# Performance work log

Measured on AMD Instinct MI355X. Metric: run time of the kernel, lower is better.

The kernel has to match this reference:

```python
import jax, jax.numpy as jnp
import numpy as np

L, B, C, H = 1024, 8, 1024, 16
D = C // H  # 64


def setup_inputs() -> dict:
    key = jax.random.key(0)
    ks = jax.random.split(key, 8)
    hidden_states = jax.random.normal(ks[0], (L, B, C), dtype=jnp.float32)
    rotary_pos_emb = jax.random.uniform(ks[1], (L, D // 2), dtype=jnp.float32) * 10.0
    attention_mask = jax.random.randint(ks[2], (B, L, L), 0, 2) > 0
    s = 1.0 / np.sqrt(C)
    Wqkv = jax.random.uniform(ks[3], (3 * C, C), dtype=jnp.float32, minval=-s, maxval=s)
    bqkv = jax.random.uniform(ks[4], (3 * C,), dtype=jnp.float32, minval=-s, maxval=s)
    Wo = jax.random.uniform(ks[5], (C, C), dtype=jnp.float32, minval=-s, maxval=s)
    bo = jax.random.uniform(ks[6], (C,), dtype=jnp.float32, minval=-s, maxval=s)
    return {"hidden_states": hidden_states, "rotary_pos_emb": rotary_pos_emb,
            "attention_mask": attention_mask, "Wqkv": Wqkv, "bqkv": bqkv, "Wo": Wo, "bo": bo}


def _rotate_half(x):
    # interleaved pairs: [-x1, x0, -x3, x2, ...]
    x2 = x.reshape(*x.shape[:-1], -1, 2)
    return jnp.stack((-x2[..., 1], x2[..., 0]), axis=-1).reshape(x.shape)


def reference(hidden_states, rotary_pos_emb, attention_mask, Wqkv, bqkv, Wo, bo):
    Lx, Bx, Cx = hidden_states.shape
    # QKV projection: (L,B,3C) -> (3,B,L,H,D)
    qkv = hidden_states @ Wqkv.T + bqkv
    qkv = qkv.reshape(Lx, Bx, 3, H, D).transpose(2, 1, 0, 3, 4)
    q, k, v = qkv[0], qkv[1], qkv[2]  # (B, L, H, D)
    # RoPE: freqs (L, D/2) -> cos/sin (1, L, 1, D) via duplication
    rpe = rotary_pos_emb[None] if rotary_pos_emb.ndim == 2 else rotary_pos_emb
    cos = jnp.concatenate([jnp.cos(rpe), jnp.cos(rpe)], axis=-1)[:, :, None, :]
    sin = jnp.concatenate([jnp.sin(rpe), jnp.sin(rpe)], axis=-1)[:, :, None, :]
    q = q * cos + _rotate_half(q) * sin
    k = k * cos + _rotate_half(k) * sin
    # (B, H, L, D)
    q = q.transpose(0, 2, 1, 3)
    k = k.transpose(0, 2, 1, 3)
    v = v.transpose(0, 2, 1, 3)
    scale = 1.0 / jnp.sqrt(jnp.asarray(D, dtype=q.dtype))
    scores = jnp.einsum('bhqd,bhkd->bhqk', q, k) * scale
    # torch SDPA bool mask: True = attend, False = masked
    scores = jnp.where(attention_mask[:, None, :, :], scores, jnp.finfo(scores.dtype).min)
    attn = jax.nn.softmax(scores, axis=-1)
    out = jnp.einsum('bhqk,bhkd->bhqd', attn, v)  # (B, H, L, D)
    out = out.transpose(2, 0, 1, 3).reshape(Lx, Bx, Cx)  # (L, B, C)
    return out @ Wo.T + bo
```

## Files before the change

### kernel.cpp

```cpp
#include <hip/hip_runtime.h>
#include <hip/hip_bf16.h>

typedef short bf16x8 __attribute__((ext_vector_type(8)));
typedef short bf16x4 __attribute__((ext_vector_type(4)));
typedef float f32x4 __attribute__((ext_vector_type(4)));
typedef unsigned int u32;
typedef unsigned long long u64;

#define GLD_LDS16(gp, lp) \
  __builtin_amdgcn_global_load_lds((const __attribute__((address_space(1))) u32*)(gp), \
                                   (__attribute__((address_space(3))) u32*)(lp), 16, 0, 0)

__device__ __forceinline__ short f2bf(float f) {
  u32 u = __builtin_bit_cast(u32, f);
  u = (u + 0x7fffu + ((u >> 16) & 1u)) >> 16;
  return (short)u;
}

__device__ __forceinline__ u32 pack2_bf16(float a, float b) {
#if __has_builtin(__builtin_amdgcn_cvt_pk_bf16_f32)
  typedef __bf16 bf16v2 __attribute__((ext_vector_type(2)));
  bf16v2 r = __builtin_amdgcn_cvt_pk_bf16_f32(a, b);
  return __builtin_bit_cast(u32, r);
#else
  u32 r;
  asm("v_cvt_pk_bf16_f32 %0, %1, %2" : "=v"(r) : "v"(a), "v"(b));
  return r;
#endif
}

__device__ __forceinline__ float exp2_fast(float x) {
#if __has_builtin(__builtin_amdgcn_exp2f)
  return __builtin_amdgcn_exp2f(x);
#else
  return exp2f(x);
#endif
}

__global__ __launch_bounds__(256) void prep_all(
    const int* __restrict__ m, u64* __restrict__ maskb,
    const float* __restrict__ hs, const float* __restrict__ wqkv,
    const float* __restrict__ wo, short* __restrict__ xb,
    short* __restrict__ wqkvb, short* __restrict__ wob,
    const float* __restrict__ rpe, float* __restrict__ cosT,
    float* __restrict__ sinT) {
  int b = blockIdx.x;
  if (b < 32768) {
    int i = b * 256 + threadIdx.x;
    u64 bm = __ballot(m[i] != 0);
    if ((threadIdx.x & 63) == 0) maskb[i >> 6] = bm;
    return;
  }
  b -= 32768;
  if (b < 12288) {
    const float* in;
    short* out;
    int base;
    if (b < 8192) {
      in = hs; out = xb; base = b * 1024;
    } else if (b < 8192 + 3072) {
      in = wqkv; out = wqkvb; base = (b - 8192) * 1024;
    } else {
      in = wo; out = wob; base = (b - 11264) * 1024;
    }
    int i = base + threadIdx.x * 4;
    float4 v = *(const float4*)(in + i);
    short4 o;
    o.x = f2bf(v.x); o.y = f2bf(v.y); o.z = f2bf(v.z); o.w = f2bf(v.w);
    *(short4*)(out + i) = o;
    return;
  }
  b -= 12288;
  int i = b * 256 + threadIdx.x;
  float v = rpe[i];
  cosT[i] = cosf(v);
  sinT[i] = sinf(v);
}

__global__ __launch_bounds__(512, 2) void gemm_qkv(
    const short* __restrict__ Xb, const short* __restrict__ Wb,
    const float* __restrict__ bqkv, const float* __restrict__ cosT,
    const float* __restrict__ sinT, short* __restrict__ qb,
    short* __restrict__ kbuf, short* __restrict__ vbuf) {
  __shared__ short lds[3][24576];
  const int tid = threadIdx.x;
  const int wid = tid >> 6, lane = tid & 63;
  const int g = lane >> 4, c = lane & 15;
  const int wm = wid >> 2, wn = wid & 3;
  const int bid = blockIdx.y * 12 + blockIdx.x;
  const int swz = (bid & 7) * 96 + (bid >> 3);
  const int m0 = (swz / 12) * 128, n0 = (swz % 12) * 256;

  f32x4 acc[4][4];
#pragma unroll
  for (int i = 0; i < 4; i++)
#pragma unroll
    for (int j = 0; j < 4; j++) acc[i][j] = (f32x4){0.f, 0.f, 0.f, 0.f};

  const int trow = tid >> 3;
  const int gch = ((tid & 7) ^ (trow & 7)) * 8;
  const short* Ag = Xb + (long)(m0 + trow) * 1024 + gch;
  const short* Bg = Wb + (long)(n0 + trow) * 1024 + gch;
  const int lo = tid * 8;

  const int fA = (wm * 64 + c) * 64;
  const int fB = 8192 + (wn * 64 + c) * 64;
  const int ck0 = (g ^ (c & 7)) * 8;

#define QKV_STG_P0(bs, ko) do { \
    GLD_LDS16(Ag + (ko),             &lds[bs][lo]); \
    GLD_LDS16(Ag + (ko) + 64 * 1024, &lds[bs][4096 + lo]); \
    GLD_LDS16(Bg + (ko),             &lds[bs][8192 + lo]); \
  } while (0)
#define QKV_STG_P1(bs, ko) do { \
    GLD_LDS16(Bg + (ko) + 64 * 1024,  &lds[bs][12288 + lo]); \
    GLD_LDS16(Bg + (ko) + 128 * 1024, &lds[bs][16384 + lo]); \
    GLD_LDS16(Bg + (ko) + 192 * 1024, &lds[bs][20480 + lo]); \
  } while (0)

  QKV_STG_P0(0, 0);  QKV_STG_P1(0, 0);
  QKV_STG_P0(1, 64); QKV_STG_P1(1, 64);
  asm volatile("s_waitcnt vmcnt(6)" ::: "memory");
  __builtin_amdgcn_s_barrier();

  int bc = 0;
  for (int kt = 0; kt < 16; ++kt) {
    const short* Bf = &lds[bc][0];
    const int bs = (bc + 2 >= 3) ? bc - 1 : bc + 2;
    const int ko2 = (kt + 2) * 64;
    bf16x8 af[4], bfr[4];

#pragma unroll
    for (int mf = 0; mf < 4; mf++) af[mf] = *(const bf16x8*)&Bf[fA + mf * 1024 + ck0];
#pragma unroll
    for (int nf = 0; nf < 4; nf++) bfr[nf] = *(const bf16x8*)&Bf[fB + nf * 1024 + ck0];
    if (kt < 14) QKV_STG_P0(bs, ko2);
    __builtin_amdgcn_s_barrier();
    asm volatile("s_waitcnt lgkmcnt(0)" ::: "memory");
    __builtin_amdgcn_sched_barrier(0);
    __builtin_amdgcn_s_setprio(1);
#pragma unroll
    for (int mf = 0; mf < 4; mf++)
#pragma unroll
      for (int nf = 0; nf < 4; nf++)
        acc[mf][nf] = __builtin_amdgcn_mfma_f32_16x16x32_bf16(bfr[nf], af[mf], acc[mf][nf], 0, 0, 0);
    __builtin_amdgcn_s_setprio(0);
    __builtin_amdgcn_s_barrier();

#pragma unroll
    for (int mf = 0; mf < 4; mf++) af[mf] = *(const bf16x8*)&Bf[fA + mf * 1024 + (ck0 ^ 32)];
#pragma unroll
    for (int nf = 0; nf < 4; nf++) bfr[nf] = *(const bf16x8*)&Bf[fB + nf * 1024 + (ck0 ^ 32)];
    if (kt < 14) QKV_STG_P1(bs, ko2);
    __builtin_amdgcn_s_barrier();
    asm volatile("s_waitcnt lgkmcnt(0)" ::: "memory");
    __builtin_amdgcn_sched_barrier(0);
    __builtin_amdgcn_s_setprio(1);
#pragma unroll
    for (int mf = 0; mf < 4; mf++)
#pragma unroll
      for (int nf = 0; nf < 4; nf++)
        acc[mf][nf] = __builtin_amdgcn_mfma_f32_16x16x32_bf16(bfr[nf], af[mf], acc[mf][nf], 0, 0, 0);
    __builtin_amdgcn_s_setprio(0);
    if (kt < 14) {
      asm volatile("s_waitcnt vmcnt(6)" ::: "memory");
    } else if (kt == 14) {
      asm volatile("s_waitcnt vmcnt(0)" ::: "memory");
    }
    __builtin_amdgcn_s_barrier();
    bc = (bc + 1 == 3) ? 0 : bc + 1;
  }
#undef QKV_STG_P0
#undef QKV_STG_P1

  for (int jt = 0; jt < 4; jt++) {
    const int chan = n0 + wn * 64 + jt * 16 + g * 4;
    const int three = chan >> 10;
    const int hh = (chan >> 6) & 15;
    const int d = chan & 63;
    const float4 bq = *(const float4*)&bqkv[chan];
    for (int i = 0; i < 4; i++) {
      const int r = m0 + wm * 64 + i * 16 + c;
      const int l = r >> 3, b = r & 7;
      float v0 = acc[i][jt][0] + bq.x;
      float v1 = acc[i][jt][1] + bq.y;
      float v2 = acc[i][jt][2] + bq.z;
      float v3 = acc[i][jt][3] + bq.w;
      const long doff = ((long)(b * 16 + hh) * 1024 + l) * 64 + d;
      if (three == 2) {
        uint2 o = {pack2_bf16(v0, v1), pack2_bf16(v2, v3)};
        *(uint2*)&vbuf[doff] = o;
      } else {
        const float4 cs = *(const float4*)&cosT[l * 32 + (d & 31)];
        const float4 sn = *(const float4*)&sinT[l * 32 + (d & 31)];
        float e0 = v0 * cs.x - v1 * sn.x;
        float o0 = v1 * cs.y + v0 * sn.y;
        float e1 = v2 * cs.z - v3 * sn.z;
        float o1 = v3 * cs.w + v2 * sn.w;
        short* dst;
        if (three == 0) {
          const float S = 0.18033688011f;
          e0 *= S; o0 *= S; e1 *= S; o1 *= S;
          dst = qb;
        } else {
          dst = kbuf;
        }
        uint2 o = {pack2_bf16(e0, o0), pack2_bf16(e1, o1)};
        *(uint2*)&dst[doff] = o;
      }
    }
  }
}

__global__ __launch_bounds__(256) void transpose_v(const short* __restrict__ vbuf,
                                                   short* __restrict__ vTb) {
  __shared__ short T[64 * 72];
  const int bh = blockIdx.y;
  const int l0 = blockIdx.x * 64;
  const int t = threadIdx.x;
  const int row = t >> 3;
  const int cc = (t & 7) * 8;
  const short* src = vbuf + ((long)bh * 1024 + l0) * 64;
  for (int p = 0; p < 2; p++) {
    int lr = row + p * 32;
    *(bf16x8*)&T[lr * 72 + cc] = *(const bf16x8*)&src[(long)lr * 64 + cc];
  }
  __syncthreads();
  short* dst = vTb + (long)bh * 64 * 1024 + l0;
  for (int p = 0; p < 2; p++) {
    int d = row + p * 32;
    bf16x8 v;
    for (int j = 0; j < 8; j++) v[j] = T[(cc + j) * 72 + d];
    *(bf16x8*)&dst[(long)d * 1024 + cc] = v;
  }
}

__global__ __launch_bounds__(256, 5) void flash_attn(
    const short* __restrict__ qb, const short* __restrict__ kbuf,
    const short* __restrict__ vTb, const u64* __restrict__ maskb,
    short* __restrict__ attno) {
  __shared__ short K0[64 * 64], K1[64 * 64];
  __shared__ short V0[64 * 64], V1[64 * 64];
  const int t = threadIdx.x;
  const int wid = t >> 6, lane = t & 63;
  const int g = lane >> 4, c = lane & 15;
  const int bid = blockIdx.y * 16 + blockIdx.x;
  const int swz = (bid & 7) * 256 + (bid >> 3);
  const int q0 = (swz & 15) * 64;
  const int bh = swz >> 4;
  const int b = bh >> 4;
  const int h = bh & 15;
  const long qoff = (long)bh * 1024 * 64;
  const int qrow = q0 + wid * 16 + c;

  bf16x8 aq0, aq1;
  {
    const short* qp = qb + qoff + (long)qrow * 64;
    aq0 = *(const bf16x8*)(qp + g * 8);
    aq1 = *(const bf16x8*)(qp + 32 + g * 8);
  }

  f32x4 Od[4];
  for (int i = 0; i < 4; i++) Od[i] = (f32x4){0.f, 0.f, 0.f, 0.f};
  f32x4 Ld = (f32x4){0.f, 0.f, 0.f, 0.f};
  float m_run = -1e30f;

  bf16x8 avOnes8;
  {
    union { bf16x8 v; u32 u[4]; } av;
    u32 o1 = (c == 0) ? 0x3F803F80u : 0u;
    av.u[0] = av.u[1] = av.u[2] = av.u[3] = o1;
    avOnes8 = av.v;
  }

  const u64* mrow = maskb + ((long)b * 1024 + qrow) * 16;
  const short* Kg = kbuf + qoff;
  const short* Vg = vTb + qoff;

  const int l8 = lane >> 3, l7 = lane & 7;
  const int sr = wid * 16 + l8;
  const int sch = ((l7 ^ l8) & 7) * 8;
  const int r1 = wid * 16 + l8;
  const int r2 = r1 + 8;
  const int kp1 = (r1 & 32) | (((r1 & 15) >> 2) << 3) | (((r1 >> 4) & 1) << 2) | (r1 & 3);
  const int kp2 = (r2 & 32) | (((r2 & 15) >> 2) << 3) | (((r2 >> 4) & 1) << 2) | (r2 & 3);

  const int ck0 = g ^ (c & 7);
  const int kOff0 = c * 64 + ck0 * 8;
  const int kOff1 = c * 64 + (ck0 ^ 4) * 8;
  int vOff32[2];
  for (int kg = 0; kg < 2; kg++)
    vOff32[kg] = c * 64 + (((kg * 4 + g) ^ (c & 7)) * 8);

#define STAGE(KD, VD, ktn) do { \
    GLD_LDS16(Kg + (long)((ktn) + kp1) * 64 + sch,      &KD[(wid * 16) * 64]); \
    GLD_LDS16(Kg + (long)((ktn) + kp2) * 64 + sch,      &KD[(wid * 16 + 8) * 64]); \
    GLD_LDS16(Vg + (long)sr * 1024 + (ktn) + sch,       &VD[(wid * 16) * 64]); \
    GLD_LDS16(Vg + (long)(sr + 8) * 1024 + (ktn) + sch, &VD[(wid * 16 + 8) * 64]); \
  } while (0)

#define TILE(KB, VB, KP, VP, ki) do { \
    u64 mw = mrow[ki]; \
    __syncthreads(); \
    STAGE(KP, VP, (((ki) + 1) & 15) * 64); \
    f32x4 z[4]; \
    for (int nt = 0; nt < 4; nt++) { \
      bf16x8 bk0 = *(const bf16x8*)&KB[kOff0 + nt * 1024]; \
      bf16x8 bk1 = *(const bf16x8*)&KB[kOff1 + nt * 1024]; \
      f32x4 zz = (f32x4){0.f, 0.f, 0.f, 0.f}; \
      zz = __builtin_amdgcn_mfma_f32_16x16x32_bf16(bk0, aq0, zz, 0, 0, 0); \
      zz = __builtin_amdgcn_mfma_f32_16x16x32_bf16(bk1, aq1, zz, 0, 0, 0); \
      z[nt] = zz; \
    } \
    float mx = fmaxf(fmaxf(fmaxf(z[0][0], z[0][1]), fmaxf(z[0][2], z[0][3])), \
                     fmaxf(fmaxf(z[1][0], z[1][1]), fmaxf(z[1][2], z[1][3]))); \
    mx = fmaxf(mx, fmaxf(fmaxf(fmaxf(z[2][0], z[2][1]), fmaxf(z[2][2], z[2][3])), \
                         fmaxf(fmaxf(z[3][0], z[3][1]), fmaxf(z[3][2], z[3][3])))); \
    if (__ballot(mx > m_run + 8.f)) { \
      mx = fmaxf(mx, __shfl_xor(mx, 16, 64)); \
      mx = fmaxf(mx, __shfl_xor(mx, 32, 64)); \
      float mnew = fmaxf(m_run, mx); \
      float al = exp2_fast(m_run - mnew); \
      for (int dt = 0; dt < 4; dt++) { \
        Od[dt][0] *= al; Od[dt][1] *= al; Od[dt][2] *= al; Od[dt][3] *= al; \
      } \
      Ld[0] *= al; \
      m_run = mnew; \
    } \
    for (int kg = 0; kg < 2; kg++) { \
      union { bf16x8 v; u32 u[4]; } pu; \
      for (int ntp = 0; ntp < 2; ntp++) { \
        const int nt = kg * 2 + ntp; \
        u32 m4 = (u32)(mw >> (kg * 32 + g * 8 + ntp * 4)) & 0xFu; \
        u32 mlo = ((m4 & 1u) ? 0xFFFFu : 0u) | ((m4 & 2u) ? 0xFFFF0000u : 0u); \
        u32 mhi = ((m4 & 4u) ? 0xFFFFu : 0u) | ((m4 & 8u) ? 0xFFFF0000u : 0u); \
        float p0 = exp2_fast(z[nt][0] - m_run); \
        float p1 = exp2_fast(z[nt][1] - m_run); \
        float p2 = exp2_fast(z[nt][2] - m_run); \
        float p3 = exp2_fast(z[nt][3] - m_run); \
        pu.u[ntp * 2 + 0] = pack2_bf16(p0, p1) & mlo; \
        pu.u[ntp * 2 + 1] = pack2_bf16(p2, p3) & mhi; \
      } \
      Ld = __builtin_amdgcn_mfma_f32_16x16x32_bf16(avOnes8, pu.v, Ld, 0, 0, 0); \
      for (int dt = 0; dt < 4; dt++) { \
        bf16x8 av = *(const bf16x8*)&VB[vOff32[kg] + dt * 1024]; \
        Od[dt] = __builtin_amdgcn_mfma_f32_16x16x32_bf16(av, pu.v, Od[dt], 0, 0, 0); \
      } \
    } \
  } while (0)

  STAGE(K0, V0, 0);
  for (int ki = 0; ki < 16; ki += 2) {
    TILE(K0, V0, K1, V1, ki);
    TILE(K1, V1, K0, V0, ki + 1);
  }
#undef TILE
#undef STAGE

  float lsum = __shfl(Ld[0], c, 64);
  float inv = 1.f / lsum;
  long rbase = ((long)qrow * 8 + b) * 1024 + h * 64 + g * 4;
  for (int dt = 0; dt < 4; dt++) {
    union { bf16x4 v; u32 u[2]; } o;
    o.u[0] = pack2_bf16(Od[dt][0] * inv, Od[dt][1] * inv);
    o.u[1] = pack2_bf16(Od[dt][2] * inv, Od[dt][3] * inv);
    *(bf16x4*)&attno[rbase + dt * 16] = o.v;
  }
}

__global__ __launch_bounds__(256, 4) void gemm_out(
    const short* __restrict__ Ab, const short* __restrict__ Wob,
    const float* __restrict__ bo, float* __restrict__ out) {
  __shared__ short Ash[2][128 * 32];
  __shared__ short Bsh[2][128 * 32];
  const int tid = threadIdx.x;
  const int wid = tid >> 6, lane = tid & 63;
  const int g = lane >> 4, c = lane & 15;
  const int wm = wid >> 1, wn = wid & 1;
  const int bid = blockIdx.y * 8 + blockIdx.x;
  const int swz = (bid & 7) * 64 + (bid >> 3);
  const int m0 = (swz >> 3) * 128, n0 = (swz & 7) * 128;

  f32x4 acc[4][4];
  for (int i = 0; i < 4; i++)
    for (int j = 0; j < 4; j++) acc[i][j] = (f32x4){0.f, 0.f, 0.f, 0.f};

  const int srow = lane >> 2;
  const int scol = ((lane & 3) ^ ((lane >> 3) & 3)) * 8;
  const short* AgL = Ab + (long)(m0 + wid * 32 + srow) * 1024 + scol;
  const short* BgL = Wob + (long)(n0 + wid * 32 + srow) * 1024 + scol;
  const int dst0 = (wid * 32) * 32;
  const int dst1 = (wid * 32 + 16) * 32;
  const int ck = g ^ ((c >> 1) & 3);

#define OUT_STAGE(PA, PB, nko) do { \
    GLD_LDS16(AgL + (nko), &(PA)[dst0]); \
    GLD_LDS16(AgL + (nko) + 16 * 1024, &(PA)[dst1]); \
    GLD_LDS16(BgL + (nko), &(PB)[dst0]); \
    GLD_LDS16(BgL + (nko) + 16 * 1024, &(PB)[dst1]); \
  } while (0)

#define OUT_COMPUTE(CA, CB) do { \
    bf16x8 af[4], bfr[4]; \
    for (int i = 0; i < 4; i++) \
      af[i] = *(const bf16x8*)&(CA)[(wm * 64 + i * 16 + c) * 32 + ck * 8]; \
    for (int j = 0; j < 4; j++) \
      bfr[j] = *(const bf16x8*)&(CB)[(wn * 64 + j * 16 + c) * 32 + ck * 8]; \
    for (int i = 0; i < 4; i++) \
      for (int j = 0; j < 4; j++) \
        acc[i][j] = __builtin_amdgcn_mfma_f32_16x16x32_bf16(af[i], bfr[j], acc[i][j], 0, 0, 0); \
  } while (0)

  OUT_STAGE(Ash[0], Bsh[0], 0);
  __syncthreads();
  for (int kt = 0; kt < 32; kt += 2) {
    OUT_STAGE(Ash[1], Bsh[1], (kt + 1) * 32);
    OUT_COMPUTE(Ash[0], Bsh[0]);
    __syncthreads();
    if (kt + 2 < 32) OUT_STAGE(Ash[0], Bsh[0], (kt + 2) * 32);
    OUT_COMPUTE(Ash[1], Bsh[1]);
    __syncthreads();
  }
#undef OUT_STAGE
#undef OUT_COMPUTE

  for (int jt = 0; jt < 4; jt++) {
    const int j = n0 + wn * 64 + jt * 16 + c;
    const float bias = bo[j];
    for (int i = 0; i < 4; i++) {
      const int rbase = m0 + wm * 64 + i * 16 + g * 4;
      for (int reg = 0; reg < 4; reg++)
        out[(long)(rbase + reg) * 1024 + j] = acc[i][jt][reg] + bias;
    }
  }
}

extern "C" void kernel_launch(void* const* d_in, const int* in_sizes, int n_in,
                              void* d_out, int out_size, void* d_ws, size_t ws_size,
                              hipStream_t stream) {
  const float* hs = (const float*)d_in[0];
  const float* rpe = (const float*)d_in[1];
  const int* amask = (const int*)d_in[2];
  const float* Wqkv = (const float*)d_in[3];
  const float* bqkv = (const float*)d_in[4];
  const float* Wo = (const float*)d_in[5];
  const float* bo = (const float*)d_in[6];
  float* out = (float*)d_out;

  char* ws = (char*)d_ws;
  auto alloc = [&](size_t bytes) {
    char* p = ws;
    ws += (bytes + 255) & ~(size_t)255;
    return p;
  };
  short* Xb = (short*)alloc(8192LL * 1024 * 2);
  short* Wqkvb = (short*)alloc(3072LL * 1024 * 2);
  short* Wob = (short*)alloc(1024LL * 1024 * 2);
  float* cosT = (float*)alloc(1024 * 32 * 4);
  float* sinT = (float*)alloc(1024 * 32 * 4);
  u64* maskb = (u64*)alloc(8LL * 1024 * 16 * 8);
  short* qb = (short*)alloc(128LL * 1024 * 64 * 2);
  short* kbuf = (short*)alloc(128LL * 1024 * 64 * 2);
  short* vbuf = (short*)alloc(128LL * 1024 * 64 * 2);
  short* vTb = (short*)alloc(128LL * 1024 * 64 * 2);
  short* attno = (short*)alloc(8192LL * 1024 * 2);

  prep_all<<<45184, 256, 0, stream>>>(amask, maskb, hs, Wqkv, Wo, Xb, Wqkvb, Wob,
                                      rpe, cosT, sinT);
  gemm_qkv<<<dim3(12, 64), 512, 0, stream>>>(Xb, Wqkvb, bqkv, cosT, sinT, qb, kbuf, vbuf);
  transpose_v<<<dim3(16, 128), 256, 0, stream>>>(vbuf, vTb);
  flash_attn<<<dim3(16, 128), 256, 0, stream>>>(qb, kbuf, vTb, maskb, attno);
  gemm_out<<<dim3(8, 64), 256, 0, stream>>>(attno, Wob, bo, out);
}
```

Before: 311.4 us.

## Restructure QKV and output GEMM main loops with register-prefetched fragments and triple buffering

The QKV GEMM loop now double-buffers fragments in registers. It reads the second K-half while issuing MFMAs on the first, then waits once per tile, barriers, issues the next global-to-LDS stage, and prefetches the next tile's first-half fragments. This drops from several barriers per tile to one. The output GEMM moves from a two-stage to a three-stage LDS ring with register-prefetched fragments and split MFMA groups, and its launch bounds drop to 3 blocks per CU to fit the larger LDS. Each tile now waits on vmcnt(0), so global-load latency is less hidden, and occupancy drops for the output GEMM.

```diff
diff --git a/kernel.cpp b/kernel.cpp
--- a/kernel.cpp
+++ b/kernel.cpp
@@ -107,71 +107,62 @@
   const int fB = 8192 + (wn * 64 + c) * 64;
   const int ck0 = (g ^ (c & 7)) * 8;
 
-#define QKV_STG_P0(bs, ko) do { \
-    GLD_LDS16(Ag + (ko),             &lds[bs][lo]); \
-    GLD_LDS16(Ag + (ko) + 64 * 1024, &lds[bs][4096 + lo]); \
-    GLD_LDS16(Bg + (ko),             &lds[bs][8192 + lo]); \
-  } while (0)
-#define QKV_STG_P1(bs, ko) do { \
+#define QKV_STG(bs, ko) do { \
+    GLD_LDS16(Ag + (ko),              &lds[bs][lo]); \
+    GLD_LDS16(Ag + (ko) + 64 * 1024,  &lds[bs][4096 + lo]); \
+    GLD_LDS16(Bg + (ko),              &lds[bs][8192 + lo]); \
     GLD_LDS16(Bg + (ko) + 64 * 1024,  &lds[bs][12288 + lo]); \
     GLD_LDS16(Bg + (ko) + 128 * 1024, &lds[bs][16384 + lo]); \
     GLD_LDS16(Bg + (ko) + 192 * 1024, &lds[bs][20480 + lo]); \
   } while (0)
 
-  QKV_STG_P0(0, 0);  QKV_STG_P1(0, 0);
-  QKV_STG_P0(1, 64); QKV_STG_P1(1, 64);
+  QKV_STG(0, 0);
+  QKV_STG(1, 64);
   asm volatile("s_waitcnt vmcnt(6)" ::: "memory");
   __builtin_amdgcn_s_barrier();
 
-  int bc = 0;
+  bf16x8 fa[2][4], fb[2][4];
+#pragma unroll
+  for (int mf = 0; mf < 4; mf++) fa[0][mf] = *(const bf16x8*)&lds[0][fA + mf * 1024 + ck0];
+#pragma unroll
+  for (int nf = 0; nf < 4; nf++) fb[0][nf] = *(const bf16x8*)&lds[0][fB + nf * 1024 + ck0];
+
+#pragma unroll
   for (int kt = 0; kt < 16; ++kt) {
-    const short* Bf = &lds[bc][0];
-    const int bs = (bc + 2 >= 3) ? bc - 1 : bc + 2;
-    const int ko2 = (kt + 2) * 64;
-    bf16x8 af[4], bfr[4];
-
-#pragma unroll
-    for (int mf = 0; mf < 4; mf++) af[mf] = *(const bf16x8*)&Bf[fA + mf * 1024 + ck0];
-#pragma unroll
-    for (int nf = 0; nf < 4; nf++) bfr[nf] = *(const bf16x8*)&Bf[fB + nf * 1024 + ck0];
-    if (kt < 14) QKV_STG_P0(bs, ko2);
-    __builtin_amdgcn_s_barrier();
-    asm volatile("s_waitcnt lgkmcnt(0)" ::: "memory");
+    const short* Bf = &lds[kt % 3][0];
+#pragma unroll
+    for (int mf = 0; mf < 4; mf++) fa[1][mf] = *(const bf16x8*)&Bf[fA + mf * 1024 + (ck0 ^ 32)];
+#pragma unroll
+    for (int nf = 0; nf < 4; nf++) fb[1][nf] = *(const bf16x8*)&Bf[fB + nf * 1024 + (ck0 ^ 32)];
     __builtin_amdgcn_sched_barrier(0);
     __builtin_amdgcn_s_setprio(1);
 #pragma unroll
     for (int mf = 0; mf < 4; mf++)
 #pragma unroll
       for (int nf = 0; nf < 4; nf++)
-        acc[mf][nf] = __builtin_amdgcn_mfma_f32_16x16x32_bf16(bfr[nf], af[mf], acc[mf][nf], 0, 0, 0);
+        acc[mf][nf] = __builtin_amdgcn_mfma_f32_16x16x32_bf16(fb[0][nf], fa[0][mf], acc[mf][nf], 0, 0, 0);
     __builtin_amdgcn_s_setprio(0);
-    __builtin_amdgcn_s_barrier();
-
-#pragma unroll
-    for (int mf = 0; mf < 4; mf++) af[mf] = *(const bf16x8*)&Bf[fA + mf * 1024 + (ck0 ^ 32)];
-#pragma unroll
-    for (int nf = 0; nf < 4; nf++) bfr[nf] = *(const bf16x8*)&Bf[fB + nf * 1024 + (ck0 ^ 32)];
-    if (kt < 14) QKV_STG_P1(bs, ko2);
-    __builtin_amdgcn_s_barrier();
-    asm volatile("s_waitcnt lgkmcnt(0)" ::: "memory");
     __builtin_amdgcn_sched_barrier(0);
+    if (kt < 15) {
+      asm volatile("s_waitcnt vmcnt(0)" ::: "memory");
+      __builtin_amdgcn_s_barrier();
+      if (kt < 14) QKV_STG((kt + 2) % 3, (kt + 2) * 64);
+      const short* Bn = &lds[(kt + 1) % 3][0];
+#pragma unroll
+      for (int mf = 0; mf < 4; mf++) fa[0][mf] = *(const bf16x8*)&Bn[fA + mf * 1024 + ck0];
+#pragma unroll
+      for (int nf = 0; nf < 4; nf++) fb[0][nf] = *(const bf16x8*)&Bn[fB + nf * 1024 + ck0];
+      __builtin_amdgcn_sched_barrier(0);
+    }
     __builtin_amdgcn_s_setprio(1);
 #pragma unroll
     for (int mf = 0; mf < 4; mf++)
 #pragma unroll
       for (int nf = 0; nf < 4; nf++)
-        acc[mf][nf] = __builtin_amdgcn_mfma_f32_16x16x32_bf16(bfr[nf], af[mf], acc[mf][nf], 0, 0, 0);
+        acc[mf][nf] = __builtin_amdgcn_mfma_f32_16x16x32_bf16(fb[1][nf], fa[1][mf], acc[mf][nf], 0, 0, 0);
     __builtin_amdgcn_s_setprio(0);
-    if (kt < 14) {
-      asm volatile("s_waitcnt vmcnt(6)" ::: "memory");
-    } else if (kt == 14) {
-      asm volatile("s_waitcnt vmcnt(0)" ::: "memory");
-    }
-    __builtin_amdgcn_s_barrier();
-    bc = (bc + 1 == 3) ? 0 : bc + 1;
-  }
-#undef QKV_STG_P0
-#undef QKV_STG_P1
+  }
+#undef QKV_STG
 
   for (int jt = 0; jt < 4; jt++) {
     const int chan = n0 + wn * 64 + jt * 16 + g * 4;
@@ -368,11 +359,11 @@
   }
 }
 
-__global__ __launch_bounds__(256, 4) void gemm_out(
+__global__ __launch_bounds__(256, 3) void gemm_out(
     const short* __restrict__ Ab, const short* __restrict__ Wob,
     const float* __restrict__ bo, float* __restrict__ out) {
-  __shared__ short Ash[2][128 * 32];
-  __shared__ short Bsh[2][128 * 32];
+  __shared__ short Ash[3][4096];
+  __shared__ short Bsh[3][4096];
   const int tid = threadIdx.x;
   const int wid = tid >> 6, lane = tid & 63;
   const int g = lane >> 4, c = lane & 15;
@@ -382,7 +373,9 @@
   const int m0 = (swz >> 3) * 128, n0 = (swz & 7) * 128;
 
   f32x4 acc[4][4];
+#pragma unroll
   for (int i = 0; i < 4; i++)
+#pragma unroll
     for (int j = 0; j < 4; j++) acc[i][j] = (f32x4){0.f, 0.f, 0.f, 0.f};
 
   const int srow = lane >> 2;
@@ -393,36 +386,59 @@
   const int dst1 = (wid * 32 + 16) * 32;
   const int ck = g ^ ((c >> 1) & 3);
 
-#define OUT_STAGE(PA, PB, nko) do { \
-    GLD_LDS16(AgL + (nko), &(PA)[dst0]); \
-    GLD_LDS16(AgL + (nko) + 16 * 1024, &(PA)[dst1]); \
-    GLD_LDS16(BgL + (nko), &(PB)[dst0]); \
-    GLD_LDS16(BgL + (nko) + 16 * 1024, &(PB)[dst1]); \
+#define OUT_STG(bs, ko) do { \
+    GLD_LDS16(AgL + (ko), &Ash[bs][dst0]); \
+    GLD_LDS16(AgL + (ko) + 16 * 1024, &Ash[bs][dst1]); \
+    GLD_LDS16(BgL + (ko), &Bsh[bs][dst0]); \
+    GLD_LDS16(BgL + (ko) + 16 * 1024, &Bsh[bs][dst1]); \
   } while (0)
 
-#define OUT_COMPUTE(CA, CB) do { \
-    bf16x8 af[4], bfr[4]; \
-    for (int i = 0; i < 4; i++) \
-      af[i] = *(const bf16x8*)&(CA)[(wm * 64 + i * 16 + c) * 32 + ck * 8]; \
-    for (int j = 0; j < 4; j++) \
-      bfr[j] = *(const bf16x8*)&(CB)[(wn * 64 + j * 16 + c) * 32 + ck * 8]; \
-    for (int i = 0; i < 4; i++) \
-      for (int j = 0; j < 4; j++) \
-        acc[i][j] = __builtin_amdgcn_mfma_f32_16x16x32_bf16(af[i], bfr[j], acc[i][j], 0, 0, 0); \
-  } while (0)
-
-  OUT_STAGE(Ash[0], Bsh[0], 0);
-  __syncthreads();
-  for (int kt = 0; kt < 32; kt += 2) {
-    OUT_STAGE(Ash[1], Bsh[1], (kt + 1) * 32);
-    OUT_COMPUTE(Ash[0], Bsh[0]);
-    __syncthreads();
-    if (kt + 2 < 32) OUT_STAGE(Ash[0], Bsh[0], (kt + 2) * 32);
-    OUT_COMPUTE(Ash[1], Bsh[1]);
-    __syncthreads();
-  }
-#undef OUT_STAGE
-#undef OUT_COMPUTE
+  OUT_STG(0, 0);
+  OUT_STG(1, 32);
+  asm volatile("s_waitcnt vmcnt(4)" ::: "memory");
+  __builtin_amdgcn_s_barrier();
+
+  bf16x8 af[2][4], bfr[2][4];
+#pragma unroll
+  for (int i = 0; i < 4; i++)
+    af[0][i] = *(const bf16x8*)&Ash[0][(wm * 64 + i * 16 + c) * 32 + ck * 8];
+#pragma unroll
+  for (int j = 0; j < 4; j++)
+    bfr[0][j] = *(const bf16x8*)&Bsh[0][(wn * 64 + j * 16 + c) * 32 + ck * 8];
+
+#pragma unroll
+  for (int kt = 0; kt < 32; ++kt) {
+    const int cur = kt & 1, nxt = cur ^ 1;
+    __builtin_amdgcn_s_setprio(1);
+#pragma unroll
+    for (int i = 0; i < 2; i++)
+#pragma unroll
+      for (int j = 0; j < 4; j++)
+        acc[i][j] = __builtin_amdgcn_mfma_f32_16x16x32_bf16(af[cur][i], bfr[cur][j], acc[i][j], 0, 0, 0);
+    __builtin_amdgcn_s_setprio(0);
+    __builtin_amdgcn_sched_barrier(0);
+    if (kt < 31) {
+      asm volatile("s_waitcnt vmcnt(0)" ::: "memory");
+      __builtin_amdgcn_s_barrier();
+      if (kt < 30) OUT_STG((kt + 2) % 3, (kt + 2) * 32);
+      const int bn = (kt + 1) % 3;
+#pragma unroll
+      for (int i = 0; i < 4; i++)
+        af[nxt][i] = *(const bf16x8*)&Ash[bn][(wm * 64 + i * 16 + c) * 32 + ck * 8];
+#pragma unroll
+      for (int j = 0; j < 4; j++)
+        bfr[nxt][j] = *(const bf16x8*)&Bsh[bn][(wn * 64 + j * 16 + c) * 32 + ck * 8];
+      __builtin_amdgcn_sched_barrier(0);
+    }
+    __builtin_amdgcn_s_setprio(1);
+#pragma unroll
+    for (int i = 2; i < 4; i++)
+#pragma unroll
+      for (int j = 0; j < 4; j++)
+        acc[i][j] = __builtin_amdgcn_mfma_f32_16x16x32_bf16(af[cur][i], bfr[cur][j], acc[i][j], 0, 0, 0);
+    __builtin_amdgcn_s_setprio(0);
+  }
+#undef OUT_STG
 
   for (int jt = 0; jt < 4; jt++) {
     const int j = n0 + wn * 64 + jt * 16 + c;
```

New measurement: 304.3 us. 1.02x faster.
